# Optimization experiments

Measured on AMD Instinct MI355X. Metric: run time of the kernel, lower is better.

Reference implementation:

```python
import jax, jax.numpy as jnp
import numpy as np
from jax import lax

B, C, H, W = 16, 256, 128, 128
MAX_ROOMS = 10

def _conv(x, w, b):
    y = lax.conv_general_dilated(x, w, window_strides=(1, 1), padding='SAME',
                                 dimension_numbers=('NCHW', 'OIHW', 'NCHW'))
    return y + b[None, :, None, None]

def setup_inputs() -> dict:
    key = jax.random.key(0)
    ks = jax.random.split(key, 16)
    def w(k, shape, fan_in):
        return jax.random.normal(k, shape, jnp.float32) * (1.0 / np.sqrt(fan_in))
    inp = {
        'features': jax.random.normal(ks[0], (B, C, H, W), jnp.float32),
        'conv1_w': w(ks[1], (C // 2, C, 3, 3), C * 9),
        'conv1_b': jnp.zeros((C // 2,), jnp.float32),
        'conv2_w': w(ks[2], (MAX_ROOMS, C // 2, 3, 3), (C // 2) * 9),
        'conv2_b': jnp.zeros((MAX_ROOMS,), jnp.float32),
        'lin1_w': w(ks[3], (256, C * 64), C * 64),
        'lin1_b': jnp.zeros((256,), jnp.float32),
        'lin2_w': w(ks[4], (128, 256), 256),
        'lin2_b': jnp.zeros((128,), jnp.float32),
        'adj1_w': w(ks[5], (64, 256), 256),
        'adj1_b': jnp.zeros((64,), jnp.float32),
        'adj2_w': w(ks[6], (32, 64), 64),
        'adj2_b': jnp.zeros((32,), jnp.float32),
        'adj3_w': w(ks[7], (1, 32), 32),
        'adj3_b': jnp.zeros((1,), jnp.float32),
    }
    return inp

def reference(features, conv1_w, conv1_b, conv2_w, conv2_b,
              lin1_w, lin1_b, lin2_w, lin2_b,
              adj1_w, adj1_b, adj2_w, adj2_b, adj3_w, adj3_b):
    # room detector: conv -> relu -> conv -> sigmoid
    h = jax.nn.relu(_conv(features, conv1_w, conv1_b))
    room_maps = jax.nn.sigmoid(_conv(h, conv2_w, conv2_b))  # [B, max_rooms, H, W]

    # room features: adaptive avg pool to 8x8 (exact since H,W divisible by 8)
    b, c = features.shape[0], features.shape[1]
    pooled = features.reshape(b, c, 8, H // 8, 8, W // 8).mean(axis=(3, 5))  # [B,C,8,8]
    flat = pooled.reshape(b, c * 64)
    feat = jax.nn.relu(flat @ lin1_w.T + lin1_b) @ lin2_w.T + lin2_b  # [B,128]

    # adjacency: original loop uses the SAME pair_feat=cat([feat,feat]) for every (i,j),
    # so compute one prob per batch row and broadcast to all off-diagonal entries.
    pair = jnp.concatenate([feat, feat], axis=-1)  # [B,256]
    a = jax.nn.relu(pair @ adj1_w.T + adj1_b)
    a = jax.nn.relu(a @ adj2_w.T + adj2_b)
    p = jax.nn.sigmoid(a @ adj3_w.T + adj3_b)  # [B,1]
    off_diag = 1.0 - jnp.eye(MAX_ROOMS, dtype=features.dtype)
    adjacency = p[:, :, None] * off_diag[None]  # [B, max_rooms, max_rooms]

    return room_maps, feat, adjacency
```

## Files before the change

### kernel.cpp

```cpp
#include <hip/hip_runtime.h>

#define HH 128
#define WW 128
#define FEAT_OFF 2621440ull
#define ADJ_OFF  2623488ull

typedef __bf16 bf16x8 __attribute__((ext_vector_type(8)));
typedef float  f32x4  __attribute__((ext_vector_type(4)));
typedef float  f32x16 __attribute__((ext_vector_type(16)));

__device__ __forceinline__ unsigned short f2bf(float f) {
  unsigned int u = __float_as_uint(f);
  unsigned int r = ((u >> 16) & 1u) + 0x7fffu;
  return (unsigned short)((u + r) >> 16);
}
__device__ __forceinline__ void gl_lds16(const void* g, void* l) {
  __builtin_amdgcn_global_load_lds((const __attribute__((address_space(1))) unsigned int*)g,
                                   (__attribute__((address_space(3))) unsigned int*)l, 16, 0, 0);
}
__device__ __forceinline__ int SW(int r) { return (r ^ (r >> 2)) & 3; }

#define FENCE() asm volatile("" ::: "memory")
#define BARRIER() do { FENCE(); __builtin_amdgcn_s_barrier(); FENCE(); } while (0)
#define LBAR() do { asm volatile("s_waitcnt lgkmcnt(0)" ::: "memory"); __builtin_amdgcn_s_barrier(); FENCE(); } while (0)

__global__ void nhwc_kernel(const float* __restrict__ F, unsigned short* __restrict__ Xn,
                            float* __restrict__ part,
                            const float* __restrict__ w1, const float* __restrict__ w2,
                            unsigned short* __restrict__ W1t, unsigned short* __restrict__ W2t,
                            unsigned short* __restrict__ zp) {
  __shared__ __align__(16) unsigned short tile[16384];
  __shared__ float pl[1024];
  int t = threadIdx.x, bi = blockIdx.x;
  if (bi < 1152) {
    int id = bi * 256 + t;
    if (id < 2048) zp[id] = 0;
    if (id < 294912) {
      int ci = id & 255, co = (id >> 8) & 127, dxy = id >> 15;
      int dy = dxy / 3, dx = dxy - 3 * dy;
      W1t[id] = f2bf(w1[((co * 256 + ci) * 3 + dy) * 3 + dx]);
    }
    if (id < 18432) {
      int ci = id & 127, co = (id >> 7) & 15, dxy = id >> 11;
      int dy = dxy / 3, dx = dxy - 3 * dy;
      W2t[id] = (co < 10) ? f2bf(w2[((co * 128 + ci) * 3 + dy) * 3 + dx]) : (unsigned short)0;
    }
  }
  int chalf = bi & 1, y = (bi >> 1) & 127, b = bi >> 8;
  int c0 = chalf * 128;
  int cp = t >> 2, xq = t & 3;
  const float* rowA = F + (((size_t)(b * 256 + c0 + cp * 2)) * HH + y) * WW + xq * 32;
  const float* rowB = rowA + (size_t)HH * WW;
  unsigned int* tw = (unsigned int*)tile;
  float s00 = 0.f, s01 = 0.f, s10 = 0.f, s11 = 0.f;
#pragma unroll
  for (int jj = 0; jj < 8; ++jj) {
    float4 va = *(const float4*)(rowA + jj * 4);
    float4 vb = *(const float4*)(rowB + jj * 4);
    float av[4] = {va.x, va.y, va.z, va.w};
    float bv[4] = {vb.x, vb.y, vb.z, vb.w};
#pragma unroll
    for (int e = 0; e < 4; ++e) {
      int xl = jj * 4 + e;
      int x = xq * 32 + xl;
      if (xl < 16) { s00 += av[e]; s10 += bv[e]; } else { s01 += av[e]; s11 += bv[e]; }
      unsigned int word = (unsigned int)f2bf(av[e]) | ((unsigned int)f2bf(bv[e]) << 16);
      tw[x * 64 + (((cp >> 2) ^ (x & 15)) << 2) + (cp & 3)] = word;
    }
  }
  pl[(cp * 2 + 0) * 8 + xq * 2 + 0] = s00;
  pl[(cp * 2 + 0) * 8 + xq * 2 + 1] = s01;
  pl[(cp * 2 + 1) * 8 + xq * 2 + 0] = s10;
  pl[(cp * 2 + 1) * 8 + xq * 2 + 1] = s11;
  __syncthreads();
  int x = t >> 1, h = t & 1;
  unsigned short* dst = Xn + ((((size_t)b * HH + y) * WW) + x) * 256 + c0;
#pragma unroll
  for (int k = 0; k < 8; ++k) {
    int s = h * 8 + k;
    *(uint4*)(dst + s * 8) = *(const uint4*)(tile + x * 128 + ((s ^ (x & 15)) << 3));
  }
  *(float4*)&part[((((size_t)b * 128 + y) * 2) + chalf) * 1024 + t * 4] = *(const float4*)&pl[t * 4];
}

__global__ void pool3_kernel(const float* __restrict__ part, float* __restrict__ pooled,
                             float* __restrict__ pooledT) {
  int bi = blockIdx.x, t = threadIdx.x;
  int py = bi & 7, chalf = (bi >> 3) & 1, b = bi >> 4;
#pragma unroll
  for (int q = 0; q < 4; ++q) {
    int i = q * 256 + t;
    float s = 0.f;
#pragma unroll
    for (int yy = 0; yy < 16; ++yy)
      s += part[((((size_t)b * 128 + py * 16 + yy) * 2) + chalf) * 1024 + i];
    int ch = i >> 3, px = i & 7;
    float v = s * (1.f / 256.f);
    int flat = (chalf * 128 + ch) * 64 + py * 8 + px;
    pooled[(size_t)b * 16384 + flat] = v;
    pooledT[(size_t)flat * 16 + b] = v;
  }
}

__global__ __launch_bounds__(512) void conv1_kernel(const unsigned short* __restrict__ X,
                                                    const unsigned short* __restrict__ Wt,
                                                    const float* __restrict__ bias,
                                                    unsigned short* __restrict__ Hout,
                                                    const unsigned short* __restrict__ zp) {
  extern __shared__ __align__(16) unsigned short smem[];
  const int t = threadIdx.x, l = t & 63, w = t >> 6;
  int bid = (blockIdx.x & 7) * 64 + (blockIdx.x >> 3);
  const int b = bid >> 5, y0 = (bid & 31) * 4;
  const int lane31 = l & 31, lh = l >> 5;
  const int yloc = w >> 1, xh = w & 1, xoff = xh * 64;

  f32x16 acc[2][4];
#pragma unroll
  for (int i = 0; i < 2; ++i)
#pragma unroll
    for (int j = 0; j < 4; ++j)
#pragma unroll
      for (int e = 0; e < 16; ++e) acc[i][j][e] = 0.f;

  auto issue_group = [&](int p, int i0, int i1, int bufsel) {
    int dy = p >> 3, cb = p & 7;
    unsigned short* buf = smem + bufsel * 30720;
    for (int i = i0; i < i1; ++i) {
      int c = w + 8 * i;
      if (c >= 60) break;
      const unsigned short* g;
      if (c < 36) {
        int air = c / 9, jj = c - air * 9;
        int er = jj * 16 + (l >> 2);
        int xin = er - 1;
        int row = y0 - 1 + dy + air;
        if (row >= 0 && row < HH && xin >= 0 && xin < WW && er < 130) {
          int kq = (l & 3) ^ SW(er);
          g = X + (((size_t)b * HH + row) * WW + xin) * 256 + cb * 32 + kq * 8;
        } else g = zp + l * 8;
      } else {
        int cc = c - 36;
        int dxi = cc >> 3, jj = cc & 7;
        int co = jj * 16 + (l >> 2);
        int kq = (l & 3) ^ SW(co);
        g = Wt + (((size_t)(dy * 3 + dxi)) * 128 + co) * 256 + cb * 32 + kq * 8;
      }
      gl_lds16(g, buf + c * 512);
    }
  };

  issue_group(0, 0, 8, 0);

  for (int p = 0; p < 24; ++p) {
    const unsigned short* buf = smem + (p & 1) * 30720;
    const unsigned short* Ab = buf + yloc * 4608;
    const unsigned short* Bb = buf + 18432;
    const int nsel = (p + 1) & 1;

    if (p < 23) issue_group(p + 1, 0, 3, nsel);
    FENCE();
    if (p < 23) asm volatile("s_waitcnt vmcnt(3)" ::: "memory");
    else        asm volatile("s_waitcnt vmcnt(0)" ::: "memory");
    BARRIER();

#pragma unroll
    for (int dx = 0; dx < 3; ++dx) {
      if (p < 23) {
        if (dx == 1)      issue_group(p + 1, 3, 6, nsel);
        else if (dx == 2) issue_group(p + 1, 6, 8, nsel);
      }
      bf16x8 a[2][2], bb[4][2];
#pragma unroll
      for (int tm = 0; tm < 2; ++tm)
#pragma unroll
        for (int ks = 0; ks < 2; ++ks) {
          int er = xoff + tm * 32 + lane31 + dx;
          int slot = (ks * 2 + lh) ^ SW(er);
          a[tm][ks] = *(const bf16x8*)(Ab + er * 32 + slot * 8);
        }
#pragma unroll
      for (int tn = 0; tn < 4; ++tn)
#pragma unroll
        for (int ks = 0; ks < 2; ++ks) {
          int co = tn * 32 + lane31;
          int slot = (ks * 2 + lh) ^ SW(co);
          bb[tn][ks] = *(const bf16x8*)(Bb + dx * 4096 + co * 32 + slot * 8);
        }
      __builtin_amdgcn_s_setprio(1);
#pragma unroll
      for (int ks = 0; ks < 2; ++ks)
#pragma unroll
        for (int tm = 0; tm < 2; ++tm)
#pragma unroll
          for (int tn = 0; tn < 4; ++tn)
            acc[tm][tn] = __builtin_amdgcn_mfma_f32_32x32x16_bf16(a[tm][ks], bb[tn][ks], acc[tm][tn], 0, 0, 0);
      __builtin_amdgcn_s_setprio(0);
    }
    BARRIER();
  }

  unsigned short* E = smem;
  for (int r = 0; r < 2; ++r) {
    if (xh == r) {
#pragma unroll
      for (int tn = 0; tn < 4; ++tn) {
        int co = tn * 32 + lane31;
        float bv = bias[co];
#pragma unroll
        for (int tm = 0; tm < 2; ++tm)
#pragma unroll
          for (int rr = 0; rr < 16; ++rr) {
            int row = (rr & 3) + 8 * (rr >> 2) + 4 * lh;
            int xl = tm * 32 + row;
            E[yloc * 8704 + xl * 136 + co] = f2bf(fmaxf(acc[tm][tn][rr] + bv, 0.f));
          }
      }
    }
    LBAR();
#pragma unroll
    for (int k = 0; k < 8; ++k) {
      int idx = k * 512 + t;
      int yl = idx >> 10, rem = idx & 1023;
      int xl = rem >> 4, oct = rem & 15;
      const uint4 v = *(const uint4*)(E + yl * 8704 + xl * 136 + oct * 8);
      size_t g = (((size_t)b * HH + y0 + yl) * WW + r * 64 + xl) * 128 + oct * 8;
      *(uint4*)(Hout + g) = v;
    }
    LBAR();
  }
}

__global__ __launch_bounds__(256) void conv2_kernel(const unsigned short* __restrict__ Hn,
                                                    const unsigned short* __restrict__ Wt,
                                                    const float* __restrict__ bias,
                                                    float* __restrict__ rmaps,
                                                    const unsigned short* __restrict__ zp) {
  extern __shared__ __align__(16) unsigned short smem[];
  const int t = threadIdx.x, l = t & 63, w = t >> 6;
  int bid = (blockIdx.x & 7) * 64 + (blockIdx.x >> 3);
  const int b = bid >> 5, y0 = (bid & 31) * 4;
  const int ko = l >> 4, r0 = l & 15;
  const int yloc = w;

  f32x4 acc[8];
#pragma unroll
  for (int i = 0; i < 8; ++i) acc[i] = {0.f, 0.f, 0.f, 0.f};

  auto stage = [&](int cb, int bufsel) {
    unsigned short* buf = smem + bufsel * 32256;
    for (int c = w; c < 63; c += 4) {
      const unsigned short* g;
      if (c < 54) {
        int air = c / 9, jj = c - air * 9;
        int er = jj * 16 + (l >> 2);
        int xin = er - 1;
        int row = y0 - 1 + air;
        if (row >= 0 && row < HH && xin >= 0 && xin < WW && er < 130) {
          int kq = (l & 3) ^ SW(er);
          g = Hn + (((size_t)b * HH + row) * WW + xin) * 128 + cb * 32 + kq * 8;
        } else g = zp + l * 8;
      } else {
        int tap = c - 54;
        int co = l >> 2;
        int kq = (l & 3) ^ SW(co);
        g = Wt + ((size_t)tap * 16 + co) * 128 + cb * 32 + kq * 8;
      }
      gl_lds16(g, buf + c * 512);
    }
  };

  stage(0, 0);
  for (int p = 0; p < 4; ++p) {
    if (p < 3) {
      stage(p + 1, (p + 1) & 1);
      FENCE();
      if (w < 3) asm volatile("s_waitcnt vmcnt(16)" ::: "memory");
      else       asm volatile("s_waitcnt vmcnt(15)" ::: "memory");
    } else {
      FENCE();
      asm volatile("s_waitcnt vmcnt(0)" ::: "memory");
    }
    BARRIER();
    const unsigned short* buf = smem + (p & 1) * 32256;
#pragma unroll
    for (int dy = 0; dy < 3; ++dy) {
      const unsigned short* Ab = buf + (yloc + dy) * 4608;
#pragma unroll
      for (int dx = 0; dx < 3; ++dx) {
        int tap = dy * 3 + dx;
        bf16x8 bbf = *(const bf16x8*)(buf + (54 + tap) * 512 + r0 * 32 + ((ko ^ SW(r0)) << 3));
#pragma unroll
        for (int mf = 0; mf < 8; ++mf) {
          int er = mf * 16 + r0 + dx;
          bf16x8 a = *(const bf16x8*)(Ab + er * 32 + ((ko ^ SW(er)) << 3));
          acc[mf] = __builtin_amdgcn_mfma_f32_16x16x32_bf16(a, bbf, acc[mf], 0, 0, 0);
        }
      }
    }
    BARRIER();
  }

  int co = r0;
  if (co < 10) {
    float bv = bias[co];
    int y = y0 + yloc;
#pragma unroll
    for (int mf = 0; mf < 8; ++mf) {
      int x = mf * 16 + ko * 4;
      float4 o;
      o.x = 1.f / (1.f + __expf(-(acc[mf][0] + bv)));
      o.y = 1.f / (1.f + __expf(-(acc[mf][1] + bv)));
      o.z = 1.f / (1.f + __expf(-(acc[mf][2] + bv)));
      o.w = 1.f / (1.f + __expf(-(acc[mf][3] + bv)));
      *(float4*)&rmaps[(((size_t)b * 10 + co) * HH + y) * WW + x] = o;
    }
  }
}

__global__ void lin1_kernel(const float* __restrict__ pooledT, const float* __restrict__ w1,
                            const float* __restrict__ b1, float* __restrict__ hidden) {
  int o = blockIdx.x, t = threadIdx.x;
  f32x4 acc[4];
#pragma unroll
  for (int q = 0; q < 4; ++q) acc[q] = {0.f, 0.f, 0.f, 0.f};
  const float* wr = w1 + (size_t)o * 16384;
  for (int i0 = t * 4; i0 < 16384; i0 += 1024) {
    float4 wv = *(const float4*)&wr[i0];
    float wa[4] = {wv.x, wv.y, wv.z, wv.w};
#pragma unroll
    for (int j = 0; j < 4; ++j) {
      const float* pt = pooledT + (size_t)(i0 + j) * 16;
#pragma unroll
      for (int q = 0; q < 4; ++q) {
        f32x4 pv = *(const f32x4*)(pt + q * 4);
#pragma unroll
        for (int e = 0; e < 4; ++e) acc[q][e] += wa[j] * pv[e];
      }
    }
  }
  __shared__ float red[16][4];
#pragma unroll
  for (int q = 0; q < 4; ++q)
#pragma unroll
    for (int e = 0; e < 4; ++e) {
      float v = acc[q][e];
      for (int s = 32; s; s >>= 1) v += __shfl_down(v, s);
      if ((t & 63) == 0) red[q * 4 + e][t >> 6] = v;
    }
  __syncthreads();
  if (t < 16) {
    float v = red[t][0] + red[t][1] + red[t][2] + red[t][3] + b1[o];
    hidden[o * 16 + t] = fmaxf(v, 0.f);
  }
}

__global__ void head_kernel(const float* __restrict__ hidden,
                            const float* __restrict__ w2, const float* __restrict__ b2,
                            const float* __restrict__ a1w, const float* __restrict__ a1b,
                            const float* __restrict__ a2w, const float* __restrict__ a2b,
                            const float* __restrict__ a3w, const float* __restrict__ a3b,
                            float* __restrict__ out) {
  int b = blockIdx.x, t = threadIdx.x;
  __shared__ float hid[256], fs[128], a1[64], a2[32], pv;
  hid[t] = hidden[t * 16 + b];
  __syncthreads();
  if (t < 128) {
    float s = b2[t];
    for (int k = 0; k < 256; ++k) s += hid[k] * w2[t * 256 + k];
    fs[t] = s;
    out[FEAT_OFF + b * 128 + t] = s;
  }
  __syncthreads();
  if (t < 64) {
    float s = a1b[t];
    for (int k = 0; k < 128; ++k) s += fs[k] * (a1w[t * 256 + k] + a1w[t * 256 + 128 + k]);
    a1[t] = fmaxf(s, 0.f);
  }
  __syncthreads();
  if (t < 32) {
    float s = a2b[t];
    for (int k = 0; k < 64; ++k) s += a1[k] * a2w[t * 64 + k];
    a2[t] = fmaxf(s, 0.f);
  }
  __syncthreads();
  if (t == 0) {
    float s = a3b[0];
    for (int k = 0; k < 32; ++k) s += a2[k] * a3w[k];
    pv = 1.f / (1.f + __expf(-s));
  }
  __syncthreads();
  if (t < 100) out[ADJ_OFF + b * 100 + t] = ((t / 10) == (t % 10)) ? 0.f : pv;
}

extern "C" void kernel_launch(void* const* d_in, const int* in_sizes, int n_in,
                              void* d_out, int out_size, void* d_ws, size_t ws_size,
                              hipStream_t stream) {
  const float* F   = (const float*)d_in[0];
  const float* w1  = (const float*)d_in[1];
  const float* b1  = (const float*)d_in[2];
  const float* w2  = (const float*)d_in[3];
  const float* b2  = (const float*)d_in[4];
  const float* l1w = (const float*)d_in[5];
  const float* l1b = (const float*)d_in[6];
  const float* l2w = (const float*)d_in[7];
  const float* l2b = (const float*)d_in[8];
  const float* a1w = (const float*)d_in[9];
  const float* a1b = (const float*)d_in[10];
  const float* a2w = (const float*)d_in[11];
  const float* a2b = (const float*)d_in[12];
  const float* a3w = (const float*)d_in[13];
  const float* a3b = (const float*)d_in[14];
  float* out = (float*)d_out;
  char* ws = (char*)d_ws;

  const size_t zp_off   = 0;
  const size_t w1t_off  = 4096;
  const size_t w2t_off  = w1t_off + 589824;
  const size_t xn_off   = w2t_off + 36864;
  const size_t hn_off   = xn_off + 134217728ull;
  const size_t pool_off = hn_off + 67108864ull;
  const size_t poolT_off= pool_off + 1048576ull;
  const size_t hid_off  = poolT_off + 1048576ull;
  const size_t need     = hid_off + 16384ull;
  if (ws_size < need) return;

  unsigned short* zp  = (unsigned short*)(ws + zp_off);
  unsigned short* W1t = (unsigned short*)(ws + w1t_off);
  unsigned short* W2t = (unsigned short*)(ws + w2t_off);
  unsigned short* Xn  = (unsigned short*)(ws + xn_off);
  unsigned short* Hn  = (unsigned short*)(ws + hn_off);
  float* part    = (float*)(ws + hn_off);
  float* pooled  = (float*)(ws + pool_off);
  float* pooledT = (float*)(ws + poolT_off);
  float* hidden  = (float*)(ws + hid_off);
  (void)pooled;

  hipFuncSetAttribute((const void*)conv1_kernel, hipFuncAttributeMaxDynamicSharedMemorySize, 122880);
  hipFuncSetAttribute((const void*)conv2_kernel, hipFuncAttributeMaxDynamicSharedMemorySize, 129024);

  nhwc_kernel<<<4096, 256, 0, stream>>>(F, Xn, part, w1, w2, W1t, W2t, zp);
  pool3_kernel<<<256, 256, 0, stream>>>(part, pooled, pooledT);
  conv1_kernel<<<512, 512, 122880, stream>>>(Xn, W1t, b1, Hn, zp);
  conv2_kernel<<<512, 256, 129024, stream>>>(Hn, W2t, b2, out, zp);
  lin1_kernel<<<256, 256, 0, stream>>>(pooledT, l1w, l1b, hidden);
  head_kernel<<<16, 256, 0, stream>>>(hidden, l2w, l2b, a1w, a1b, a2w, a2b, a3w, a3b, out);
}
```

Measured before the change: 340.2 us.

## Preload conv2 weights once, reswizzle NHWC tile, drop unused pooled output

conv2 now loads all weight taps for every channel block into LDS once before the loop, and only the activation halo is double-buffered per block. This cuts redundant weight traffic per stage but raises LDS use to 144KB per block. The NHWC transpose tile gets an extra XOR term to reduce LDS bank conflicts. pool3 stops writing the unused row-major pooled array, removing one global store stream.

Result: slower. 359.6 us (+5.7%).

```diff
diff --git a/kernel.cpp b/kernel.cpp
--- a/kernel.cpp
+++ b/kernel.cpp
@@ -65,7 +65,8 @@
       int x = xq * 32 + xl;
       if (xl < 16) { s00 += av[e]; s10 += bv[e]; } else { s01 += av[e]; s11 += bv[e]; }
       unsigned int word = (unsigned int)f2bf(av[e]) | ((unsigned int)f2bf(bv[e]) << 16);
-      tw[x * 64 + (((cp >> 2) ^ (x & 15)) << 2) + (cp & 3)] = word;
+      int slot = ((cp >> 2) ^ (x & 15) ^ ((x >> 5) << 2)) & 15;
+      tw[x * 64 + (slot << 2) + (cp & 3)] = word;
     }
   }
   pl[(cp * 2 + 0) * 8 + xq * 2 + 0] = s00;
@@ -78,13 +79,13 @@
 #pragma unroll
   for (int k = 0; k < 8; ++k) {
     int s = h * 8 + k;
-    *(uint4*)(dst + s * 8) = *(const uint4*)(tile + x * 128 + ((s ^ (x & 15)) << 3));
+    int slot = (s ^ (x & 15) ^ ((x >> 5) << 2)) & 15;
+    *(uint4*)(dst + s * 8) = *(const uint4*)(tile + x * 128 + (slot << 3));
   }
   *(float4*)&part[((((size_t)b * 128 + y) * 2) + chalf) * 1024 + t * 4] = *(const float4*)&pl[t * 4];
 }
 
-__global__ void pool3_kernel(const float* __restrict__ part, float* __restrict__ pooled,
-                             float* __restrict__ pooledT) {
+__global__ void pool3_kernel(const float* __restrict__ part, float* __restrict__ pooledT) {
   int bi = blockIdx.x, t = threadIdx.x;
   int py = bi & 7, chalf = (bi >> 3) & 1, b = bi >> 4;
 #pragma unroll
@@ -95,10 +96,8 @@
     for (int yy = 0; yy < 16; ++yy)
       s += part[((((size_t)b * 128 + py * 16 + yy) * 2) + chalf) * 1024 + i];
     int ch = i >> 3, px = i & 7;
-    float v = s * (1.f / 256.f);
     int flat = (chalf * 128 + ch) * 64 + py * 8 + px;
-    pooled[(size_t)b * 16384 + flat] = v;
-    pooledT[(size_t)flat * 16 + b] = v;
+    pooledT[(size_t)flat * 16 + b] = s * (1.f / 256.f);
   }
 }
 
@@ -241,54 +240,58 @@
   const int b = bid >> 5, y0 = (bid & 31) * 4;
   const int ko = l >> 4, r0 = l & 15;
   const int yloc = w;
+  unsigned short* Wl = smem;
 
   f32x4 acc[8];
 #pragma unroll
   for (int i = 0; i < 8; ++i) acc[i] = {0.f, 0.f, 0.f, 0.f};
 
-  auto stage = [&](int cb, int bufsel) {
-    unsigned short* buf = smem + bufsel * 32256;
-    for (int c = w; c < 63; c += 4) {
+  auto stageW = [&]() {
+    for (int c = w; c < 36; c += 4) {
+      int tap = c >> 2, cb = c & 3;
+      int co = l >> 2;
+      int kq = (l & 3) ^ SW(co);
+      gl_lds16(Wt + ((size_t)tap * 16 + co) * 128 + cb * 32 + kq * 8, Wl + c * 512);
+    }
+  };
+  auto stageA = [&](int cb, int sel) {
+    unsigned short* buf = smem + 18432 + sel * 27648;
+    for (int c = w; c < 54; c += 4) {
+      int air = c / 9, jj = c - air * 9;
+      int er = jj * 16 + (l >> 2);
+      int xin = er - 1;
+      int row = y0 - 1 + air;
       const unsigned short* g;
-      if (c < 54) {
-        int air = c / 9, jj = c - air * 9;
-        int er = jj * 16 + (l >> 2);
-        int xin = er - 1;
-        int row = y0 - 1 + air;
-        if (row >= 0 && row < HH && xin >= 0 && xin < WW && er < 130) {
-          int kq = (l & 3) ^ SW(er);
-          g = Hn + (((size_t)b * HH + row) * WW + xin) * 128 + cb * 32 + kq * 8;
-        } else g = zp + l * 8;
-      } else {
-        int tap = c - 54;
-        int co = l >> 2;
-        int kq = (l & 3) ^ SW(co);
-        g = Wt + ((size_t)tap * 16 + co) * 128 + cb * 32 + kq * 8;
-      }
+      if (row >= 0 && row < HH && xin >= 0 && xin < WW && er < 130) {
+        int kq = (l & 3) ^ SW(er);
+        g = Hn + (((size_t)b * HH + row) * WW + xin) * 128 + cb * 32 + kq * 8;
+      } else g = zp + l * 8;
       gl_lds16(g, buf + c * 512);
     }
   };
 
-  stage(0, 0);
+  stageW();
+  stageA(0, 0);
+  FENCE();
+  asm volatile("s_waitcnt vmcnt(0)" ::: "memory");
+  BARRIER();
+
   for (int p = 0; p < 4; ++p) {
     if (p < 3) {
-      stage(p + 1, (p + 1) & 1);
+      stageA(p + 1, (p + 1) & 1);
       FENCE();
-      if (w < 3) asm volatile("s_waitcnt vmcnt(16)" ::: "memory");
-      else       asm volatile("s_waitcnt vmcnt(15)" ::: "memory");
-    } else {
-      FENCE();
-      asm volatile("s_waitcnt vmcnt(0)" ::: "memory");
-    }
-    BARRIER();
-    const unsigned short* buf = smem + (p & 1) * 32256;
+      if (w < 2) asm volatile("s_waitcnt vmcnt(14)" ::: "memory");
+      else       asm volatile("s_waitcnt vmcnt(13)" ::: "memory");
+      BARRIER();
+    }
+    const unsigned short* buf = smem + 18432 + (p & 1) * 27648;
 #pragma unroll
     for (int dy = 0; dy < 3; ++dy) {
       const unsigned short* Ab = buf + (yloc + dy) * 4608;
 #pragma unroll
       for (int dx = 0; dx < 3; ++dx) {
         int tap = dy * 3 + dx;
-        bf16x8 bbf = *(const bf16x8*)(buf + (54 + tap) * 512 + r0 * 32 + ((ko ^ SW(r0)) << 3));
+        bf16x8 bbf = *(const bf16x8*)(Wl + (tap * 4 + p) * 512 + r0 * 32 + ((ko ^ SW(r0)) << 3));
 #pragma unroll
         for (int mf = 0; mf < 8; ++mf) {
           int er = mf * 16 + r0 + dx;
@@ -418,8 +421,7 @@
   const size_t w2t_off  = w1t_off + 589824;
   const size_t xn_off   = w2t_off + 36864;
   const size_t hn_off   = xn_off + 134217728ull;
-  const size_t pool_off = hn_off + 67108864ull;
-  const size_t poolT_off= pool_off + 1048576ull;
+  const size_t poolT_off= hn_off + 67108864ull;
   const size_t hid_off  = poolT_off + 1048576ull;
   const size_t need     = hid_off + 16384ull;
   if (ws_size < need) return;
@@ -430,18 +432,16 @@
   unsigned short* Xn  = (unsigned short*)(ws + xn_off);
   unsigned short* Hn  = (unsigned short*)(ws + hn_off);
   float* part    = (float*)(ws + hn_off);
-  float* pooled  = (float*)(ws + pool_off);
   float* pooledT = (float*)(ws + poolT_off);
   float* hidden  = (float*)(ws + hid_off);
-  (void)pooled;
 
   hipFuncSetAttribute((const void*)conv1_kernel, hipFuncAttributeMaxDynamicSharedMemorySize, 122880);
-  hipFuncSetAttribute((const void*)conv2_kernel, hipFuncAttributeMaxDynamicSharedMemorySize, 129024);
+  hipFuncSetAttribute((const void*)conv2_kernel, hipFuncAttributeMaxDynamicSharedMemorySize, 147456);
 
   nhwc_kernel<<<4096, 256, 0, stream>>>(F, Xn, part, w1, w2, W1t, W2t, zp);
-  pool3_kernel<<<256, 256, 0, stream>>>(part, pooled, pooledT);
+  pool3_kernel<<<256, 256, 0, stream>>>(part, pooledT);
   conv1_kernel<<<512, 512, 122880, stream>>>(Xn, W1t, b1, Hn, zp);
-  conv2_kernel<<<512, 256, 129024, stream>>>(Hn, W2t, b2, out, zp);
+  conv2_kernel<<<512, 256, 147456, stream>>>(Hn, W2t, b2, out, zp);
   lin1_kernel<<<256, 256, 0, stream>>>(pooledT, l1w, l1b, hidden);
   head_kernel<<<16, 256, 0, stream>>>(hidden, l2w, l2b, a1w, a1b, a2w, a2b, a3w, a3b, out);
 }
```
